# Performance work log

Measured on AMD Instinct MI355X. Metric: run time of the kernel, lower is better.

## Reference

```python
import jax, jax.numpy as jnp
import numpy as np

V, E, H, B, S = 32000, 1024, 1024, 64, 128


def setup_inputs() -> dict:
    key = jax.random.key(0)
    ks = jax.random.split(key, 16)
    s = 0.02
    return {
        "input_seq": jax.random.randint(ks[0], (B, 1), 0, V),
        "hidden": jax.random.normal(ks[1], (1, B, H), jnp.float32),
        "cell": jax.random.normal(ks[2], (1, B, H), jnp.float32),
        "encoder_outputs": jax.random.normal(ks[3], (B, S, H), jnp.float32),
        "emb": jax.random.normal(ks[4], (V, E), jnp.float32) * s,
        "Wa_w": jax.random.normal(ks[5], (H, H), jnp.float32) * s,
        "Wa_b": jnp.zeros((H,), jnp.float32),
        "Ua_w": jax.random.normal(ks[6], (H, H), jnp.float32) * s,
        "Ua_b": jnp.zeros((H,), jnp.float32),
        "Va_w": jax.random.normal(ks[7], (1, H), jnp.float32) * s,
        "Va_b": jnp.zeros((1,), jnp.float32),
        "W_ih": jax.random.normal(ks[8], (4 * H, E + H), jnp.float32) * s,
        "W_hh": jax.random.normal(ks[9], (4 * H, H), jnp.float32) * s,
        "b_ih": jnp.zeros((4 * H,), jnp.float32),
        "b_hh": jnp.zeros((4 * H,), jnp.float32),
        "out_w": jax.random.normal(ks[10], (V, H), jnp.float32) * s,
        "out_b": jnp.zeros((V,), jnp.float32),
    }


def reference(input_seq, hidden, cell, encoder_outputs, emb, Wa_w, Wa_b, Ua_w, Ua_b,
              Va_w, Va_b, W_ih, W_hh, b_ih, b_hh, out_w, out_b):
    # embedding lookup (dropout p=0 -> identity): [B,1,E]
    embedded = emb[input_seq]
    # query = last layer hidden: [B,1,H]
    query = hidden[-1][:, None, :]
    # Bahdanau additive attention
    q_proj = query @ Wa_w.T + Wa_b                       # [B,1,H]
    k_proj = encoder_outputs @ Ua_w.T + Ua_b             # [B,S,H]
    scores = jnp.tanh(q_proj + k_proj) @ Va_w.T + Va_b   # [B,S,1]
    scores = scores[..., 0][:, None, :]                  # [B,1,S]
    weights = jax.nn.softmax(scores, axis=-1)            # [B,1,S]
    context = jnp.einsum('bqs,bsh->bqh', weights, encoder_outputs)  # [B,1,H]
    # LSTM single step on concat(embedded, context)
    x = jnp.concatenate([embedded, context], axis=2)[:, 0, :]  # [B,E+H]
    h0, c0 = hidden[0], cell[0]
    gates = x @ W_ih.T + b_ih + h0 @ W_hh.T + b_hh       # [B,4H]
    i, f, g, o = jnp.split(gates, 4, axis=-1)
    c1 = jax.nn.sigmoid(f) * c0 + jax.nn.sigmoid(i) * jnp.tanh(g)
    h1 = jax.nn.sigmoid(o) * jnp.tanh(c1)
    output = h1[:, None, :]                              # [B,1,H]
    logits = output @ out_w.T + out_b                    # [B,1,V]
    return logits, h1[None], c1[None], weights
```

## Files before the change

### kernel.cpp

```cpp
#include <hip/hip_runtime.h>
#include <hip/hip_bf16.h>

using short8 = __attribute__((ext_vector_type(8))) short;
using f32x4  = __attribute__((ext_vector_type(4))) float;

__device__ inline unsigned pk2(float lo, float hi) {
    __hip_bfloat162 h = __float22bfloat162_rn(float2{lo, hi});
    return *reinterpret_cast<unsigned*>(&h);
}
__device__ inline short8 cvt8(float4 a, float4 b) {
    union { unsigned u[4]; short8 s; } r;
    r.u[0] = pk2(a.x, a.y); r.u[1] = pk2(a.z, a.w);
    r.u[2] = pk2(b.x, b.y); r.u[3] = pk2(b.z, b.w);
    return r.s;
}
__device__ inline float ftanh(float x) {
    float e = __expf(2.f * x);
    return 1.f - 2.f / (e + 1.f);
}
__device__ inline void gload16(const void* g, void* lds) {
    __builtin_amdgcn_global_load_lds(
        (const __attribute__((address_space(1))) unsigned int*)g,
        (__attribute__((address_space(3))) unsigned int*)lds, 16, 0, 0);
}

__global__ void k_init(const int* __restrict__ idx, const float* __restrict__ emb,
                       const float* __restrict__ h0, float* __restrict__ xcat,
                       float4* __restrict__ wsz) {
    int i = blockIdx.x * blockDim.x + threadIdx.x;
    if (i < 18432) {
        float4 z = {0.f, 0.f, 0.f, 0.f};
        wsz[i] = z;
    } else if (i < 67584) {
        int j = i - 18432;
        int b = j / 768, q = j - b * 768;
        if (q < 256)
            ((float4*)(xcat + (size_t)b * 3072))[q] =
                ((const float4*)(emb + (size_t)idx[b] * 1024))[q];
        else if (q >= 512)
            ((float4*)(xcat + (size_t)b * 3072))[q] =
                ((const float4*)(h0 + (size_t)b * 1024))[q - 512];
    }
}

__global__ void k_cvt_swz(const float* __restrict__ enc, const float* __restrict__ Ua,
                          short* __restrict__ dst) {
    int i = blockIdx.x * blockDim.x + threadIdx.x;
    if (i >= 9216 * 128) return;
    int row = i >> 7, gi = i & 127;
    int seg = gi >> 3, g = gi & 7;
    const float* src = (row < 8192) ? enc + ((size_t)row << 10)
                                    : Ua + ((size_t)(row - 8192) << 10);
    const float* p = src + (seg << 6) + ((g ^ (row & 7)) << 3);
    float4 v0 = *(const float4*)p;
    float4 v1 = *(const float4*)(p + 4);
    *(short8*)&dst[(size_t)i << 3] = cvt8(v0, v1);
}

__global__ __launch_bounds__(512) void k_attn2(
    const short* __restrict__ Abf, const short* __restrict__ Bbf,
    const float* __restrict__ Uab, const float* __restrict__ Wab,
    const float* __restrict__ qp, const float* __restrict__ Va,
    float* __restrict__ scores) {
    __shared__ short As[256 * 64];
    __shared__ short Bs[128 * 64];
    const int t = threadIdx.x;
    const int l = t & 63, w = t >> 6;
    const int wm = w >> 1, wn = w & 1;
    const int lr = l & 15, lg = l >> 4;
    const int n0 = blockIdx.x * 128;
    const int r0 = blockIdx.y * 256;

    f32x4 acc[4][4];
#pragma unroll
    for (int i = 0; i < 4; ++i)
#pragma unroll
        for (int j = 0; j < 4; ++j) { f32x4 z = {0.f, 0.f, 0.f, 0.f}; acc[i][j] = z; }

    for (int seg = 0; seg < 16; ++seg) {
#pragma unroll
        for (int i = 0; i < 4; ++i) {
            int base = i * 512 + w * 64;
            int s = base + l;
            gload16(Abf + (((size_t)r0 + (s >> 3)) << 10) + (seg << 6) + ((s & 7) << 3),
                    (void*)&As[base * 8]);
            if (i < 2)
                gload16(Bbf + (((size_t)8192 + n0 + (s >> 3)) << 10) + (seg << 6) + ((s & 7) << 3),
                        (void*)&Bs[base * 8]);
        }
        __syncthreads();
#pragma unroll
        for (int kh = 0; kh < 2; ++kh) {
            short8 a[4], b[4];
#pragma unroll
            for (int i = 0; i < 4; ++i) {
                int ra = wm * 64 + i * 16 + lr;
                a[i] = *(const short8*)&As[ra * 64 + (((kh * 4 + lg) ^ (ra & 7)) << 3)];
                int rb = wn * 64 + i * 16 + lr;
                b[i] = *(const short8*)&Bs[rb * 64 + (((kh * 4 + lg) ^ (rb & 7)) << 3)];
            }
#pragma unroll
            for (int i = 0; i < 4; ++i)
#pragma unroll
                for (int j = 0; j < 4; ++j)
                    acc[i][j] = __builtin_amdgcn_mfma_f32_16x16x32_bf16(a[i], b[j], acc[i][j], 0, 0, 0);
        }
        __syncthreads();
    }

    float va[4], ub[4];
#pragma unroll
    for (int j = 0; j < 4; ++j) {
        int h = n0 + wn * 64 + j * 16 + lr;
        va[j] = Va[h];
        ub[j] = Uab[h] + Wab[h];
    }
#pragma unroll
    for (int i = 0; i < 4; ++i)
#pragma unroll
        for (int r = 0; r < 4; ++r) {
            int row = r0 + wm * 64 + i * 16 + lg * 4 + r;
            const float* qpb = qp + (size_t)(row >> 7) * 1024;
            float s = 0.f;
#pragma unroll
            for (int j = 0; j < 4; ++j) {
                int h = n0 + wn * 64 + j * 16 + lr;
                s += va[j] * ftanh(acc[i][j][r] + qpb[h] + ub[j]);
            }
            s += __shfl_xor(s, 1);
            s += __shfl_xor(s, 2);
            s += __shfl_xor(s, 4);
            s += __shfl_xor(s, 8);
            if (lr == 0) atomicAdd(scores + row, s);
        }
}

template <int EPI>
__global__ __launch_bounds__(256) void k_sgemm(
    const float* __restrict__ A, int lda,
    const float* __restrict__ B0, int ldb0,
    const float* __restrict__ B1, int ldb1, int kyB1,
    float* __restrict__ C, int ldc, int Kblk, int pstride) {
    __shared__ short As[64 * 64];
    __shared__ short Bs[64 * 64];
    const int t = threadIdx.x;
    const int l = t & 63, w = t >> 6;
    const int wm = w >> 1, wn = w & 1;
    const int lr = l & 15, lg = l >> 4;
    const int n0 = blockIdx.x * 64;
    const int ky = blockIdx.y;

    const float* Ab = A + (size_t)ky * Kblk;
    const float* Bb;
    int ldb;
    if (ky < kyB1) { Bb = B0 + (size_t)ky * Kblk; ldb = ldb0; }
    else           { Bb = B1 + (size_t)(ky - kyB1) * Kblk; ldb = ldb1; }

    f32x4 acc[2][2];
#pragma unroll
    for (int i = 0; i < 2; ++i)
#pragma unroll
        for (int j = 0; j < 2; ++j) { f32x4 z = {0.f, 0.f, 0.f, 0.f}; acc[i][j] = z; }

    for (int kt = 0; kt < Kblk; kt += 64) {
#pragma unroll
        for (int i = 0; i < 2; ++i) {
            int s = t + 256 * i, row = s >> 3, ch = s & 7;
            const float* p = Ab + (size_t)row * lda + kt + ch * 8;
            *(short8*)&As[row * 64 + ((ch ^ (row & 7)) << 3)] =
                cvt8(*(const float4*)p, *(const float4*)(p + 4));
            const float* q = Bb + (size_t)(n0 + row) * ldb + kt + ch * 8;
            *(short8*)&Bs[row * 64 + ((ch ^ (row & 7)) << 3)] =
                cvt8(*(const float4*)q, *(const float4*)(q + 4));
        }
        __syncthreads();
#pragma unroll
        for (int kh = 0; kh < 2; ++kh) {
            short8 a[2], b[2];
#pragma unroll
            for (int i = 0; i < 2; ++i) {
                int ra = wm * 32 + i * 16 + lr;
                a[i] = *(const short8*)&As[ra * 64 + (((kh * 4 + lg) ^ (ra & 7)) << 3)];
                int rb = wn * 32 + i * 16 + lr;
                b[i] = *(const short8*)&Bs[rb * 64 + (((kh * 4 + lg) ^ (rb & 7)) << 3)];
            }
#pragma unroll
            for (int i = 0; i < 2; ++i)
#pragma unroll
                for (int j = 0; j < 2; ++j)
                    acc[i][j] = __builtin_amdgcn_mfma_f32_16x16x32_bf16(a[i], b[j], acc[i][j], 0, 0, 0);
        }
        __syncthreads();
    }

    float* Cp = (EPI == 0) ? C + (size_t)ky * pstride : C;
#pragma unroll
    for (int i = 0; i < 2; ++i)
#pragma unroll
        for (int j = 0; j < 2; ++j)
#pragma unroll
            for (int r = 0; r < 4; ++r) {
                int R = wm * 32 + i * 16 + lg * 4 + r;
                int c = n0 + wn * 32 + j * 16 + lr;
                if constexpr (EPI == 1)
                    atomicAdd(&C[(size_t)R * ldc + c], acc[i][j][r]);
                else
                    Cp[(size_t)R * ldc + c] = acc[i][j][r];
            }
}

__global__ __launch_bounds__(256) void k_smctx(
    const float* __restrict__ scores, const float* __restrict__ enc,
    float* __restrict__ wout, float* __restrict__ xcat) {
    int b = blockIdx.x;
    int t = threadIdx.x;
    __shared__ float buf[128];
    __shared__ float wsb[128];
    if (t < 128) buf[t] = scores[b * 128 + t];
    __syncthreads();
    if (t < 64) buf[t] = fmaxf(buf[t], buf[t + 64]);
    __syncthreads();
    if (t < 32) buf[t] = fmaxf(buf[t], buf[t + 32]);
    __syncthreads();
    float m;
    {
        float v = buf[t & 31];
        for (int off = 16; off > 0; off >>= 1)
            v = fmaxf(v, __shfl_xor(v, off, 32));
        m = v;
    }
    __syncthreads();
    if (t < 128) wsb[t] = __expf(scores[b * 128 + t] - m);
    __syncthreads();
    if (t < 64) buf[t] = wsb[t] + wsb[t + 64];
    __syncthreads();
    if (t < 32) buf[t] += buf[t + 32];
    __syncthreads();
    float sum;
    {
        float v = buf[t & 31];
        for (int off = 16; off > 0; off >>= 1)
            v += __shfl_xor(v, off, 32);
        sum = v;
    }
    float inv = 1.f / sum;
    __syncthreads();
    if (t < 128) {
        wsb[t] *= inv;
        wout[b * 128 + t] = wsb[t];
    }
    __syncthreads();
    float acc[4] = {0.f, 0.f, 0.f, 0.f};
    for (int s = 0; s < 128; ++s) {
        float wv = wsb[s];
        const float* row = enc + ((size_t)b * 128 + s) * 1024;
#pragma unroll
        for (int j = 0; j < 4; ++j) acc[j] += wv * row[t + 256 * j];
    }
#pragma unroll
    for (int j = 0; j < 4; ++j) xcat[(size_t)b * 3072 + 1024 + t + 256 * j] = acc[j];
}

__global__ void k_lstm6(const float* __restrict__ gp, const float* __restrict__ c0,
                        const float* __restrict__ b_ih, const float* __restrict__ b_hh,
                        float* __restrict__ h1, float* __restrict__ c1) {
    int idx = blockIdx.x * blockDim.x + threadIdx.x;
    int b = idx >> 10, h = idx & 1023;
    const float* g0 = gp + (size_t)b * 4096;
    float iv = b_ih[h] + b_hh[h];
    float fv = b_ih[1024 + h] + b_hh[1024 + h];
    float gv = b_ih[2048 + h] + b_hh[2048 + h];
    float ov = b_ih[3072 + h] + b_hh[3072 + h];
#pragma unroll
    for (int p = 0; p < 6; ++p) {
        const float* g = g0 + p * 262144;
        iv += g[h];
        fv += g[1024 + h];
        gv += g[2048 + h];
        ov += g[3072 + h];
    }
    float si = 1.f / (1.f + expf(-iv));
    float sf = 1.f / (1.f + expf(-fv));
    float so = 1.f / (1.f + expf(-ov));
    float tg = tanhf(gv);
    float cc = sf * c0[idx] + si * tg;
    float hh = so * tanhf(cc);
    c1[idx] = cc;
    h1[idx] = hh;
}

__global__ void k_red4(const float* __restrict__ lp, const float* __restrict__ ob,
                       float* __restrict__ logits) {
    int i = blockIdx.x * blockDim.x + threadIdx.x;
    if (i >= 512000) return;
    int c4 = i - (i / 8000) * 8000;
    float4 s = ((const float4*)ob)[c4];
#pragma unroll
    for (int p = 0; p < 4; ++p) {
        float4 v = ((const float4*)(lp + (size_t)p * 2048000))[i];
        s.x += v.x; s.y += v.y; s.z += v.z; s.w += v.w;
    }
    ((float4*)logits)[i] = s;
}

extern "C" void kernel_launch(void* const* d_in, const int* in_sizes, int n_in,
                              void* d_out, int out_size, void* d_ws, size_t ws_size,
                              hipStream_t stream) {
    const int* idx = (const int*)d_in[0];
    const float* hidden = (const float*)d_in[1];
    const float* cell = (const float*)d_in[2];
    const float* enc = (const float*)d_in[3];
    const float* emb = (const float*)d_in[4];
    const float* Wa_w = (const float*)d_in[5];
    const float* Wa_b = (const float*)d_in[6];
    const float* Ua_w = (const float*)d_in[7];
    const float* Ua_b = (const float*)d_in[8];
    const float* Va_w = (const float*)d_in[9];
    const float* W_ih = (const float*)d_in[11];
    const float* W_hh = (const float*)d_in[12];
    const float* b_ih = (const float*)d_in[13];
    const float* b_hh = (const float*)d_in[14];
    const float* out_w = (const float*)d_in[15];
    const float* out_b = (const float*)d_in[16];

    float* out = (float*)d_out;
    float* logits = out;
    float* h1 = out + 2048000;
    float* c1 = out + 2048000 + 65536;
    float* wts = out + 2048000 + 65536 + 65536;

    float* ws = (float*)d_ws;
    float* qp = ws;
    float* scores = ws + 65536;
    float* xcat = ws + 73728;
    float* gates_p = ws + 270336;
    float* logits_p = ws + 1843200;
    short* encua_bf = (short*)(ws + 10035200);

    k_init<<<264, 256, 0, stream>>>(idx, emb, hidden, xcat, (float4*)ws);
    k_cvt_swz<<<4608, 256, 0, stream>>>(enc, Ua_w, encua_bf);
    k_sgemm<1><<<dim3(16, 8), 256, 0, stream>>>(hidden, 1024, Wa_w, 1024,
                                                nullptr, 0, 99, qp, 1024, 128, 0);
    k_attn2<<<dim3(8, 32), 512, 0, stream>>>(encua_bf, encua_bf, Ua_b, Wa_b,
                                             qp, Va_w, scores);
    k_smctx<<<64, 256, 0, stream>>>(scores, enc, wts, xcat);
    k_sgemm<0><<<dim3(64, 6), 256, 0, stream>>>(xcat, 3072, W_ih, 2048,
                                                W_hh, 1024, 4, gates_p, 4096, 512, 262144);
    k_lstm6<<<256, 256, 0, stream>>>(gates_p, cell, b_ih, b_hh, h1, c1);
    k_sgemm<0><<<dim3(500, 4), 256, 0, stream>>>(h1, 1024, out_w, 1024,
                                                 nullptr, 0, 99, logits_p, 32000, 256, 2048000);
    k_red4<<<2000, 256, 0, stream>>>(logits_p, out_b, logits);
}
```

Before: 138.3 us.

## Replace split-K output GEMM and reduction with direct bf16 MFMA vocab GEMM

The LSTM kernel now also writes h1 in bf16. A new k_vgemm kernel computes the output projection without split-K: each wave streams 16 rows of out_w straight from global memory, converts them to bf16 and runs MFMA against all 64 batch rows, adding the bias in the epilogue. This removes the 4-way partial-logits buffer, its write and re-read, and the separate reduction launch. The cost is less parallelism (500 blocks with full K each), no LDS staging, and B-tile loads that may not coalesce well.

```diff
diff --git a/kernel.cpp b/kernel.cpp
--- a/kernel.cpp
+++ b/kernel.cpp
@@ -22,6 +22,10 @@
     __builtin_amdgcn_global_load_lds(
         (const __attribute__((address_space(1))) unsigned int*)g,
         (__attribute__((address_space(3))) unsigned int*)lds, 16, 0, 0);
+}
+__device__ inline short f2b(float f) {
+    unsigned u = __float_as_uint(f);
+    return (short)((u + 0x7FFFu + ((u >> 16) & 1u)) >> 16);
 }
 
 __global__ void k_init(const int* __restrict__ idx, const float* __restrict__ emb,
@@ -209,6 +213,46 @@
             }
 }
 
+__global__ __launch_bounds__(256) void k_vgemm(
+    const short* __restrict__ Abf,
+    const float* __restrict__ B,
+    const float* __restrict__ bias,
+    float* __restrict__ C) {
+    const int t = threadIdx.x;
+    const int l = t & 63, w = t >> 6;
+    const int lr = l & 15, lg = l >> 4;
+    const int n0 = blockIdx.x * 64 + w * 16;
+
+    f32x4 acc[4];
+#pragma unroll
+    for (int i = 0; i < 4; ++i) { f32x4 z = {0.f, 0.f, 0.f, 0.f}; acc[i] = z; }
+
+    const float* bp = B + (size_t)(n0 + lr) * 1024 + lg * 8;
+    const short* ap = Abf + lr * 1024 + lg * 8;
+
+#pragma unroll 4
+    for (int k0 = 0; k0 < 1024; k0 += 32) {
+        float4 b0 = *(const float4*)(bp + k0);
+        float4 b1 = *(const float4*)(bp + k0 + 4);
+        short8 a0 = *(const short8*)(ap + k0);
+        short8 a1 = *(const short8*)(ap + k0 + 16 * 1024);
+        short8 a2 = *(const short8*)(ap + k0 + 32 * 1024);
+        short8 a3 = *(const short8*)(ap + k0 + 48 * 1024);
+        short8 bf = cvt8(b0, b1);
+        acc[0] = __builtin_amdgcn_mfma_f32_16x16x32_bf16(a0, bf, acc[0], 0, 0, 0);
+        acc[1] = __builtin_amdgcn_mfma_f32_16x16x32_bf16(a1, bf, acc[1], 0, 0, 0);
+        acc[2] = __builtin_amdgcn_mfma_f32_16x16x32_bf16(a2, bf, acc[2], 0, 0, 0);
+        acc[3] = __builtin_amdgcn_mfma_f32_16x16x32_bf16(a3, bf, acc[3], 0, 0, 0);
+    }
+
+    float bv = bias[n0 + lr];
+#pragma unroll
+    for (int i = 0; i < 4; ++i)
+#pragma unroll
+        for (int r = 0; r < 4; ++r)
+            C[(size_t)(i * 16 + lg * 4 + r) * 32000 + n0 + lr] = acc[i][r] + bv;
+}
+
 __global__ __launch_bounds__(256) void k_smctx(
     const float* __restrict__ scores, const float* __restrict__ enc,
     float* __restrict__ wout, float* __restrict__ xcat) {
@@ -263,7 +307,8 @@
 
 __global__ void k_lstm6(const float* __restrict__ gp, const float* __restrict__ c0,
                         const float* __restrict__ b_ih, const float* __restrict__ b_hh,
-                        float* __restrict__ h1, float* __restrict__ c1) {
+                        float* __restrict__ h1, float* __restrict__ c1,
+                        short* __restrict__ h1bf) {
     int idx = blockIdx.x * blockDim.x + threadIdx.x;
     int b = idx >> 10, h = idx & 1023;
     const float* g0 = gp + (size_t)b * 4096;
@@ -287,20 +332,7 @@
     float hh = so * tanhf(cc);
     c1[idx] = cc;
     h1[idx] = hh;
-}
-
-__global__ void k_red4(const float* __restrict__ lp, const float* __restrict__ ob,
-                       float* __restrict__ logits) {
-    int i = blockIdx.x * blockDim.x + threadIdx.x;
-    if (i >= 512000) return;
-    int c4 = i - (i / 8000) * 8000;
-    float4 s = ((const float4*)ob)[c4];
-#pragma unroll
-    for (int p = 0; p < 4; ++p) {
-        float4 v = ((const float4*)(lp + (size_t)p * 2048000))[i];
-        s.x += v.x; s.y += v.y; s.z += v.z; s.w += v.w;
-    }
-    ((float4*)logits)[i] = s;
+    h1bf[idx] = f2b(hh);
 }
 
 extern "C" void kernel_launch(void* const* d_in, const int* in_sizes, int n_in,
@@ -334,8 +366,8 @@
     float* scores = ws + 65536;
     float* xcat = ws + 73728;
     float* gates_p = ws + 270336;
-    float* logits_p = ws + 1843200;
-    short* encua_bf = (short*)(ws + 10035200);
+    short* h1_bf = (short*)(ws + 1843200);
+    short* encua_bf = (short*)(ws + 1908736);
 
     k_init<<<264, 256, 0, stream>>>(idx, emb, hidden, xcat, (float4*)ws);
     k_cvt_swz<<<4608, 256, 0, stream>>>(enc, Ua_w, encua_bf);
@@ -346,8 +378,6 @@
     k_smctx<<<64, 256, 0, stream>>>(scores, enc, wts, xcat);
     k_sgemm<0><<<dim3(64, 6), 256, 0, stream>>>(xcat, 3072, W_ih, 2048,
                                                 W_hh, 1024, 4, gates_p, 4096, 512, 262144);
-    k_lstm6<<<256, 256, 0, stream>>>(gates_p, cell, b_ih, b_hh, h1, c1);
-    k_sgemm<0><<<dim3(500, 4), 256, 0, stream>>>(h1, 1024, out_w, 1024,
-                                                 nullptr, 0, 99, logits_p, 32000, 256, 2048000);
-    k_red4<<<2000, 256, 0, stream>>>(logits_p, out_b, logits);
-}
+    k_lstm6<<<256, 256, 0, stream>>>(gates_p, cell, b_ih, b_hh, h1, c1, h1_bf);
+    k_vgemm<<<500, 256, 0, stream>>>(h1_bf, out_w, out_b, logits);
+}
```

Result: no change. 137.0 us (-1.0%).
